# Optimization experiments

Measured on AMD Instinct MI355X. Metric: run time of the kernel, lower is better.

Reference implementation:

```python
import jax, jax.numpy as jnp
import numpy as np

N_NODES = 19
N_T = 4096
LATENT = 512
HID = 2048
N_EDGES = 342


def setup_inputs() -> dict:
    key = jax.random.key(0)
    ks = jax.random.split(key, 16)
    s = lambda fan_in: 1.0 / np.sqrt(fan_in)
    d = {}
    d["latent_z"] = jax.random.normal(ks[0], (N_NODES, LATENT), dtype=jnp.float32)
    d["edge_idx"] = jax.random.randint(ks[1], (2, N_EDGES), 0, N_NODES, dtype=jnp.int64)
    # GIN layer 1 MLP: [LATENT -> HID -> HID]
    d["W1a"] = jax.random.uniform(ks[2], (LATENT, HID), jnp.float32, -s(LATENT), s(LATENT))
    d["b1a"] = jnp.zeros((HID,), jnp.float32)
    d["W1b"] = jax.random.uniform(ks[3], (HID, HID), jnp.float32, -s(HID), s(HID))
    d["b1b"] = jnp.zeros((HID,), jnp.float32)
    # GIN layer 2 MLP: [HID -> N_T -> N_T]
    d["W2a"] = jax.random.uniform(ks[4], (HID, N_T), jnp.float32, -s(HID), s(HID))
    d["b2a"] = jnp.zeros((N_T,), jnp.float32)
    d["W2b"] = jax.random.uniform(ks[5], (N_T, N_T), jnp.float32, -s(N_T), s(N_T))
    d["b2b"] = jnp.zeros((N_T,), jnp.float32)
    # Classifier: Linear(19*4096 -> LATENT), Linear(LATENT -> 1)
    fc_in = N_NODES * N_T
    d["Wc1"] = jax.random.uniform(ks[6], (fc_in, LATENT), jnp.float32, -s(fc_in), s(fc_in))
    d["bc1"] = jnp.zeros((LATENT,), jnp.float32)
    d["Wc2"] = jax.random.uniform(ks[7], (LATENT, 1), jnp.float32, -s(LATENT), s(LATENT))
    d["bc2"] = jnp.zeros((1,), jnp.float32)
    return d


def _gin_agg(h, edge_idx):
    # sum aggregation: message from src (row 0) to dst (row 1); eps = 0
    src, dst = edge_idx[0], edge_idx[1]
    agg = jax.ops.segment_sum(h[src], dst, num_segments=N_NODES)
    return h + agg


def reference(latent_z, edge_idx, W1a, b1a, W1b, b1b, W2a, b2a, W2b, b2b, Wc1, bc1, Wc2, bc2):
    # GINConv 1: nn((1+eps)*x + sum_j x_j), MLP = Lin->ReLU->Lin
    h = _gin_agg(latent_z, edge_idx)
    h = jax.nn.relu(h @ W1a + b1a) @ W1b + b1b
    h = jax.nn.relu(h)  # inter-layer activation (BasicGNN)
    # GINConv 2 (last layer: no trailing activation)
    h = _gin_agg(h, edge_idx)
    gin_recon_signal = jax.nn.relu(h @ W2a + b2a) @ W2b + b2b  # [19, 4096]
    flat = gin_recon_signal.reshape(N_NODES * N_T)
    dem_pred = jax.nn.sigmoid((flat @ Wc1 + bc1) @ Wc2 + bc2)  # [1]
    return (dem_pred, gin_recon_signal)
```

## Files before the change

kernel.cpp:

```cpp
#include <hip/hip_runtime.h>

#define NN 19
#define NT 4096
#define LAT 512
#define HID 2048
#define NE 342

__device__ __forceinline__ void build_M(const int* __restrict__ ei, float* sM,
                                        int* scratch, int t) {
    int* cnt = scratch;
    int* flag = scratch + NN * NN;
    if (t == 0) *flag = 0;
    for (int i = t; i < NN * NN; i += 256) cnt[i] = 0;
    __syncthreads();
    int f = 0;
    for (int i = t; i < NE; i += 256) f |= ei[2 * i + 1];
    if (f) atomicOr(flag, 1);
    __syncthreads();
    const bool i64 = (*flag == 0);
    for (int i = t; i < NE; i += 256) {
        const int s = i64 ? ei[2 * i] : ei[i];
        const int d = i64 ? ei[2 * NE + 2 * i] : ei[NE + i];
        atomicAdd(&cnt[d * NN + s], 1);
    }
    __syncthreads();
    for (int i = t; i < NN * NN; i += 256)
        sM[i] = (float)cnt[i] + ((i / NN) == (i % NN) ? 1.f : 0.f);
    __syncthreads();
}

template <int BK, int N>
__device__ __forceinline__ void gemm_inner(int t, int kc, int cb,
                                           const float* __restrict__ W,
                                           float* __restrict__ part,
                                           const float* __restrict__ sA) {
    const int k0 = kc * BK;
    const int col = cb * 1024 + 4 * t;
    const float4* __restrict__ w = (const float4*)(W + (size_t)k0 * N + col);
    float4 acc[NN];
#pragma unroll
    for (int i = 0; i < NN; ++i) acc[i] = make_float4(0.f, 0.f, 0.f, 0.f);
#pragma unroll 1
    for (int kk = 0; kk < BK; kk += 8) {
        float4 wb[8];
#pragma unroll
        for (int u = 0; u < 8; ++u) wb[u] = w[(size_t)(kk + u) * (N / 4)];
#pragma unroll
        for (int u = 0; u < 8; ++u) {
#pragma unroll
            for (int i = 0; i < NN; ++i) {
                const float av = sA[(kk + u) * 21 + i];
                acc[i].x = fmaf(av, wb[u].x, acc[i].x);
                acc[i].y = fmaf(av, wb[u].y, acc[i].y);
                acc[i].z = fmaf(av, wb[u].z, acc[i].z);
                acc[i].w = fmaf(av, wb[u].w, acc[i].w);
            }
        }
    }
    float* __restrict__ p = part + (size_t)kc * NN * N + col;
#pragma unroll
    for (int i = 0; i < NN; ++i) *(float4*)(p + (size_t)i * N) = acc[i];
}

__global__ __launch_bounds__(256) void gemm_l1a(const float* __restrict__ z,
                                                const int* __restrict__ ei,
                                                const float* __restrict__ W1a,
                                                float* __restrict__ part1) {
    __shared__ __align__(16) float sA[32 * 21];
    __shared__ __align__(16) float sZ[32 * 21];
    __shared__ float sM[NN * NN];
    __shared__ int scratch[NN * NN + 1];
    const int t = threadIdx.x, cb = blockIdx.x, kc = blockIdx.y;
    const int k0 = kc * 32;
    build_M(ei, sM, scratch, t);
    for (int idx = t; idx < NN * 32; idx += 256) {
        const int s = idx / 32, c = idx % 32;
        sZ[c * 21 + s] = z[(size_t)s * LAT + k0 + c];
    }
    __syncthreads();
    for (int idx = t; idx < NN * 32; idx += 256) {
        const int i = idx / 32, c = idx % 32;
        float acc = 0.f;
#pragma unroll
        for (int s = 0; s < NN; ++s) acc = fmaf(sM[i * NN + s], sZ[c * 21 + s], acc);
        sA[c * 21 + i] = acc;
    }
    __syncthreads();
    gemm_inner<32, HID>(t, kc, cb, W1a, part1, sA);
}

__global__ __launch_bounds__(256) void gemm_l1b(const float* __restrict__ part1,
                                                const float* __restrict__ b1a,
                                                const float* __restrict__ W1b,
                                                float* __restrict__ part2) {
    __shared__ __align__(16) float sA[64 * 21];
    const int t = threadIdx.x, cb = blockIdx.x, kc = blockIdx.y;
    const int k0 = kc * 64;
    for (int idx = t; idx < NN * 64; idx += 256) {
        const int i = idx / 64, c = idx % 64;
        const int k = k0 + c;
        float s = b1a[k];
#pragma unroll
        for (int cc = 0; cc < 16; ++cc) s += part1[((size_t)cc * NN + i) * HID + k];
        sA[c * 21 + i] = s > 0.f ? s : 0.f;
    }
    __syncthreads();
    gemm_inner<64, HID>(t, kc, cb, W1b, part2, sA);
}

__global__ __launch_bounds__(256) void gemm_l2a(const float* __restrict__ part2,
                                                const float* __restrict__ b1b,
                                                const int* __restrict__ ei,
                                                const float* __restrict__ W2a,
                                                float* __restrict__ part3) {
    __shared__ __align__(16) float sA[64 * 21];
    __shared__ __align__(16) float sZ[64 * 21];
    __shared__ float sM[NN * NN];
    __shared__ int scratch[NN * NN + 1];
    const int t = threadIdx.x, cb = blockIdx.x, kc = blockIdx.y;
    const int k0 = kc * 64;
    build_M(ei, sM, scratch, t);
    for (int idx = t; idx < NN * 64; idx += 256) {
        const int i = idx / 64, c = idx % 64;
        const int k = k0 + c;
        float s = b1b[k];
#pragma unroll
        for (int cc = 0; cc < 32; ++cc) s += part2[((size_t)cc * NN + i) * HID + k];
        sZ[c * 21 + i] = s > 0.f ? s : 0.f;
    }
    __syncthreads();
    for (int idx = t; idx < NN * 64; idx += 256) {
        const int i = idx / 64, c = idx % 64;
        float acc = 0.f;
#pragma unroll
        for (int s = 0; s < NN; ++s) acc = fmaf(sM[i * NN + s], sZ[c * 21 + s], acc);
        sA[c * 21 + i] = acc;
    }
    __syncthreads();
    gemm_inner<64, NT>(t, kc, cb, W2a, part3, sA);
}

__global__ __launch_bounds__(256) void gemm_l2b(const float* __restrict__ part3,
                                                const float* __restrict__ b2a,
                                                const float* __restrict__ W2b,
                                                float* __restrict__ part4) {
    __shared__ __align__(16) float sA[64 * 21];
    const int t = threadIdx.x, cb = blockIdx.x, kc = blockIdx.y;
    const int k0 = kc * 64;
    for (int idx = t; idx < NN * 64; idx += 256) {
        const int i = idx / 64, c = idx % 64;
        const int k = k0 + c;
        float s = b2a[k];
#pragma unroll
        for (int cc = 0; cc < 32; ++cc) s += part3[((size_t)cc * NN + i) * NT + k];
        sA[c * 21 + i] = s > 0.f ? s : 0.f;
    }
    __syncthreads();
    gemm_inner<64, NT>(t, kc, cb, W2b, part4, sA);
}

__global__ __launch_bounds__(256) void cls_out(const float* __restrict__ part4,
                                               const float* __restrict__ b2b,
                                               const float* __restrict__ Wc1,
                                               float* __restrict__ out1,
                                               float* __restrict__ partC) {
    __shared__ float sF[304];
    __shared__ __align__(16) float4 comb[128];
    const int t = threadIdx.x;
    const int k0 = blockIdx.x * 304;
    for (int e = t; e < 304; e += 256) {
        const int f = k0 + e;
        const int i = f >> 12, n = f & 4095;
        float s = b2b[n];
#pragma unroll 16
        for (int cc = 0; cc < 64; ++cc) s += part4[((size_t)cc * NN + i) * NT + n];
        sF[e] = s;
        out1[f] = s;
    }
    __syncthreads();
    const int q = t & 127, kp = t >> 7;
    const float4* __restrict__ w = (const float4*)Wc1 + (size_t)k0 * 128 + q;
    float4 acc = make_float4(0.f, 0.f, 0.f, 0.f);
#pragma unroll 1
    for (int k = kp; k < 304; k += 16) {
        float4 wb[8];
        float fv[8];
#pragma unroll
        for (int u = 0; u < 8; ++u) wb[u] = w[(size_t)(k + 2 * u) * 128];
#pragma unroll
        for (int u = 0; u < 8; ++u) fv[u] = sF[k + 2 * u];
#pragma unroll
        for (int u = 0; u < 8; ++u) {
            acc.x = fmaf(fv[u], wb[u].x, acc.x);
            acc.y = fmaf(fv[u], wb[u].y, acc.y);
            acc.z = fmaf(fv[u], wb[u].z, acc.z);
            acc.w = fmaf(fv[u], wb[u].w, acc.w);
        }
    }
    if (kp) comb[q] = acc;
    __syncthreads();
    if (!kp) {
        const float4 o = comb[q];
        acc.x += o.x; acc.y += o.y; acc.z += o.z; acc.w += o.w;
        ((float4*)partC)[(size_t)blockIdx.x * 128 + q] = acc;
    }
}

__global__ __launch_bounds__(256) void cls_reduce(const float* __restrict__ partC,
                                                  float* __restrict__ part2c) {
    const int g = blockIdx.x, t = threadIdx.x;
    float2 s = make_float2(0.f, 0.f);
#pragma unroll
    for (int c = 0; c < 16; ++c) {
        const float2 v = *(const float2*)(partC + (size_t)(g * 16 + c) * LAT + 2 * t);
        s.x += v.x; s.y += v.y;
    }
    *(float2*)(part2c + (size_t)g * LAT + 2 * t) = s;
}

__global__ __launch_bounds__(512) void cls_final(const float* __restrict__ part2c,
                                                 const float* __restrict__ bc1,
                                                 const float* __restrict__ Wc2,
                                                 const float* __restrict__ bc2,
                                                 float* __restrict__ out) {
    __shared__ float red[512];
    const int t = threadIdx.x;
    float s = bc1[t];
#pragma unroll
    for (int g = 0; g < 16; ++g) s += part2c[(size_t)g * LAT + t];
    red[t] = s * Wc2[t];
    __syncthreads();
    for (int off = 256; off > 0; off >>= 1) {
        if (t < off) red[t] += red[t + off];
        __syncthreads();
    }
    if (t == 0) out[0] = 1.f / (1.f + expf(-(red[0] + bc2[0])));
}

extern "C" void kernel_launch(void* const* d_in, const int* in_sizes, int n_in,
                              void* d_out, int out_size, void* d_ws, size_t ws_size,
                              hipStream_t stream) {
    const float* z   = (const float*)d_in[0];
    const int*   ei  = (const int*)d_in[1];
    const float* W1a = (const float*)d_in[2];
    const float* b1a = (const float*)d_in[3];
    const float* W1b = (const float*)d_in[4];
    const float* b1b = (const float*)d_in[5];
    const float* W2a = (const float*)d_in[6];
    const float* b2a = (const float*)d_in[7];
    const float* W2b = (const float*)d_in[8];
    const float* b2b = (const float*)d_in[9];
    const float* Wc1 = (const float*)d_in[10];
    const float* bc1 = (const float*)d_in[11];
    const float* Wc2 = (const float*)d_in[12];
    const float* bc2 = (const float*)d_in[13];
    float* out = (float*)d_out;
    float* ws  = (float*)d_ws;

    float* part1  = ws + 262144;
    float* part2  = ws + 1048576;
    float* part3  = ws + 2359296;
    float* part4  = ws + 4980736;
    float* partC  = ws + 10485760;
    float* part2c = ws + 10616832;

    gemm_l1a<<<dim3(2, 16), 256, 0, stream>>>(z, ei, W1a, part1);
    gemm_l1b<<<dim3(2, 32), 256, 0, stream>>>(part1, b1a, W1b, part2);
    gemm_l2a<<<dim3(4, 32), 256, 0, stream>>>(part2, b1b, ei, W2a, part3);
    gemm_l2b<<<dim3(4, 64), 256, 0, stream>>>(part3, b2a, W2b, part4);
    cls_out<<<256, 256, 0, stream>>>(part4, b2b, Wc1, out + 1, partC);
    cls_reduce<<<16, 256, 0, stream>>>(partC, part2c);
    cls_final<<<1, 512, 0, stream>>>(part2c, bc1, Wc2, bc2, out);
}
```

Measured before the change: 157.8 us.

## Fuse layer-1 GEMMs into one kernel and fold classifier reduction into last block

Layer 1's two GEMMs are merged into one 512-thread kernel. Each block computes the full aggregated input, then its 64-column slice of the first hidden layer with a K-split shuffle reduction, then feeds that slice directly into the W1b partial product. This removes the part1 round trip and one launch. The classifier's cls_reduce and cls_final kernels are folded into cls_out through an atomic counter, so the last finishing block does the final reduction and sigmoid, saving two launches. In exchange, each layer-1 block recomputes the full first-layer aggregation (32x redundant) and reads W1a column-strided. The tail also relies on a counter that is reset inside the first kernel.

```diff
diff --git a/kernel.cpp b/kernel.cpp
--- a/kernel.cpp
+++ b/kernel.cpp
@@ -7,35 +7,34 @@
 #define NE 342
 
 __device__ __forceinline__ void build_M(const int* __restrict__ ei, float* sM,
-                                        int* scratch, int t) {
+                                        int* scratch, int t, int bs) {
     int* cnt = scratch;
     int* flag = scratch + NN * NN;
     if (t == 0) *flag = 0;
-    for (int i = t; i < NN * NN; i += 256) cnt[i] = 0;
+    for (int i = t; i < NN * NN; i += bs) cnt[i] = 0;
     __syncthreads();
     int f = 0;
-    for (int i = t; i < NE; i += 256) f |= ei[2 * i + 1];
+    for (int i = t; i < NE; i += bs) f |= ei[2 * i + 1];
     if (f) atomicOr(flag, 1);
     __syncthreads();
     const bool i64 = (*flag == 0);
-    for (int i = t; i < NE; i += 256) {
+    for (int i = t; i < NE; i += bs) {
         const int s = i64 ? ei[2 * i] : ei[i];
         const int d = i64 ? ei[2 * NE + 2 * i] : ei[NE + i];
         atomicAdd(&cnt[d * NN + s], 1);
     }
     __syncthreads();
-    for (int i = t; i < NN * NN; i += 256)
+    for (int i = t; i < NN * NN; i += bs)
         sM[i] = (float)cnt[i] + ((i / NN) == (i % NN) ? 1.f : 0.f);
     __syncthreads();
 }
 
 template <int BK, int N>
-__device__ __forceinline__ void gemm_inner(int t, int kc, int cb,
+__device__ __forceinline__ void gemm_inner(int col, int kc,
                                            const float* __restrict__ W,
                                            float* __restrict__ part,
                                            const float* __restrict__ sA) {
     const int k0 = kc * BK;
-    const int col = cb * 1024 + 4 * t;
     const float4* __restrict__ w = (const float4*)(W + (size_t)k0 * N + col);
     float4 acc[NN];
 #pragma unroll
@@ -62,50 +61,90 @@
     for (int i = 0; i < NN; ++i) *(float4*)(p + (size_t)i * N) = acc[i];
 }
 
-__global__ __launch_bounds__(256) void gemm_l1a(const float* __restrict__ z,
-                                                const int* __restrict__ ei,
-                                                const float* __restrict__ W1a,
-                                                float* __restrict__ part1) {
-    __shared__ __align__(16) float sA[32 * 21];
-    __shared__ __align__(16) float sZ[32 * 21];
+__global__ __launch_bounds__(512) void gemm_l1ab(const float* __restrict__ z,
+                                                 const int* __restrict__ ei,
+                                                 const float* __restrict__ W1a,
+                                                 const float* __restrict__ b1a,
+                                                 const float* __restrict__ W1b,
+                                                 float* __restrict__ part2,
+                                                 unsigned int* __restrict__ counter) {
+    __shared__ __align__(16) float h0T[512 * 20];
+    __shared__ __align__(16) float sA[64 * 21];
     __shared__ float sM[NN * NN];
     __shared__ int scratch[NN * NN + 1];
-    const int t = threadIdx.x, cb = blockIdx.x, kc = blockIdx.y;
-    const int k0 = kc * 32;
-    build_M(ei, sM, scratch, t);
-    for (int idx = t; idx < NN * 32; idx += 256) {
-        const int s = idx / 32, c = idx % 32;
-        sZ[c * 21 + s] = z[(size_t)s * LAT + k0 + c];
-    }
-    __syncthreads();
-    for (int idx = t; idx < NN * 32; idx += 256) {
-        const int i = idx / 32, c = idx % 32;
-        float acc = 0.f;
-#pragma unroll
-        for (int s = 0; s < NN; ++s) acc = fmaf(sM[i * NN + s], sZ[c * 21 + s], acc);
-        sA[c * 21 + i] = acc;
-    }
-    __syncthreads();
-    gemm_inner<32, HID>(t, kc, cb, W1a, part1, sA);
-}
-
-__global__ __launch_bounds__(256) void gemm_l1b(const float* __restrict__ part1,
-                                                const float* __restrict__ b1a,
-                                                const float* __restrict__ W1b,
-                                                float* __restrict__ part2) {
-    __shared__ __align__(16) float sA[64 * 21];
-    const int t = threadIdx.x, cb = blockIdx.x, kc = blockIdx.y;
-    const int k0 = kc * 64;
-    for (int idx = t; idx < NN * 64; idx += 256) {
-        const int i = idx / 64, c = idx % 64;
-        const int k = k0 + c;
-        float s = b1a[k];
-#pragma unroll
-        for (int cc = 0; cc < 16; ++cc) s += part1[((size_t)cc * NN + i) * HID + k];
-        sA[c * 21 + i] = s > 0.f ? s : 0.f;
-    }
-    __syncthreads();
-    gemm_inner<64, HID>(t, kc, cb, W1b, part2, sA);
+    const int t = threadIdx.x;
+    const int kc = blockIdx.x;
+    if (kc == 0 && t == 0) *counter = 0u;
+    build_M(ei, sM, scratch, t, 512);
+    {
+        float zv[NN];
+#pragma unroll
+        for (int s = 0; s < NN; ++s) zv[s] = z[(size_t)s * LAT + t];
+#pragma unroll
+        for (int i = 0; i < NN; ++i) {
+            float a = 0.f;
+#pragma unroll
+            for (int s = 0; s < NN; ++s) a = fmaf(sM[i * NN + s], zv[s], a);
+            h0T[t * 20 + i] = a;
+        }
+    }
+    __syncthreads();
+    {
+        const int c = t >> 3, jp = t & 7;
+        const int k = kc * 64 + c;
+        float acc[NN];
+#pragma unroll
+        for (int i = 0; i < NN; ++i) acc[i] = 0.f;
+#pragma unroll 1
+        for (int jj = 0; jj < 64; jj += 8) {
+            float wv[8];
+#pragma unroll
+            for (int u = 0; u < 8; ++u)
+                wv[u] = W1a[(size_t)(8 * (jj + u) + jp) * HID + k];
+#pragma unroll
+            for (int u = 0; u < 8; ++u) {
+                const float* hr = h0T + (8 * (jj + u) + jp) * 20;
+                const float4 a0 = *(const float4*)(hr);
+                const float4 a1 = *(const float4*)(hr + 4);
+                const float4 a2 = *(const float4*)(hr + 8);
+                const float4 a3 = *(const float4*)(hr + 12);
+                const float4 a4 = *(const float4*)(hr + 16);
+                const float wu = wv[u];
+                acc[0]  = fmaf(a0.x, wu, acc[0]);
+                acc[1]  = fmaf(a0.y, wu, acc[1]);
+                acc[2]  = fmaf(a0.z, wu, acc[2]);
+                acc[3]  = fmaf(a0.w, wu, acc[3]);
+                acc[4]  = fmaf(a1.x, wu, acc[4]);
+                acc[5]  = fmaf(a1.y, wu, acc[5]);
+                acc[6]  = fmaf(a1.z, wu, acc[6]);
+                acc[7]  = fmaf(a1.w, wu, acc[7]);
+                acc[8]  = fmaf(a2.x, wu, acc[8]);
+                acc[9]  = fmaf(a2.y, wu, acc[9]);
+                acc[10] = fmaf(a2.z, wu, acc[10]);
+                acc[11] = fmaf(a2.w, wu, acc[11]);
+                acc[12] = fmaf(a3.x, wu, acc[12]);
+                acc[13] = fmaf(a3.y, wu, acc[13]);
+                acc[14] = fmaf(a3.z, wu, acc[14]);
+                acc[15] = fmaf(a3.w, wu, acc[15]);
+                acc[16] = fmaf(a4.x, wu, acc[16]);
+                acc[17] = fmaf(a4.y, wu, acc[17]);
+                acc[18] = fmaf(a4.z, wu, acc[18]);
+            }
+        }
+#pragma unroll
+        for (int i = 0; i < NN; ++i) {
+            float v = acc[i];
+            v += __shfl_down(v, 1);
+            v += __shfl_down(v, 2);
+            v += __shfl_down(v, 4);
+            if (jp == 0) {
+                const float r = v + b1a[k];
+                sA[c * 21 + i] = r > 0.f ? r : 0.f;
+            }
+        }
+    }
+    __syncthreads();
+    gemm_inner<64, HID>(4 * t, kc, W1b, part2, sA);
 }
 
 __global__ __launch_bounds__(256) void gemm_l2a(const float* __restrict__ part2,
@@ -119,7 +158,7 @@
     __shared__ int scratch[NN * NN + 1];
     const int t = threadIdx.x, cb = blockIdx.x, kc = blockIdx.y;
     const int k0 = kc * 64;
-    build_M(ei, sM, scratch, t);
+    build_M(ei, sM, scratch, t, 256);
     for (int idx = t; idx < NN * 64; idx += 256) {
         const int i = idx / 64, c = idx % 64;
         const int k = k0 + c;
@@ -137,7 +176,7 @@
         sA[c * 21 + i] = acc;
     }
     __syncthreads();
-    gemm_inner<64, NT>(t, kc, cb, W2a, part3, sA);
+    gemm_inner<64, NT>(cb * 1024 + 4 * t, kc, W2a, part3, sA);
 }
 
 __global__ __launch_bounds__(256) void gemm_l2b(const float* __restrict__ part3,
@@ -156,26 +195,33 @@
         sA[c * 21 + i] = s > 0.f ? s : 0.f;
     }
     __syncthreads();
-    gemm_inner<64, NT>(t, kc, cb, W2b, part4, sA);
-}
-
-__global__ __launch_bounds__(256) void cls_out(const float* __restrict__ part4,
-                                               const float* __restrict__ b2b,
-                                               const float* __restrict__ Wc1,
-                                               float* __restrict__ out1,
-                                               float* __restrict__ partC) {
+    gemm_inner<64, NT>(cb * 1024 + 4 * t, kc, W2b, part4, sA);
+}
+
+__global__ __launch_bounds__(256) void cls_out_tail(const float* __restrict__ part4,
+                                                    const float* __restrict__ b2b,
+                                                    const float* __restrict__ Wc1,
+                                                    const float* __restrict__ bc1,
+                                                    const float* __restrict__ Wc2,
+                                                    const float* __restrict__ bc2,
+                                                    float* __restrict__ out,
+                                                    float* __restrict__ partC,
+                                                    unsigned int* __restrict__ counter) {
     __shared__ float sF[304];
     __shared__ __align__(16) float4 comb[128];
+    __shared__ float red[128];
+    __shared__ int lastFlag;
     const int t = threadIdx.x;
     const int k0 = blockIdx.x * 304;
+    float* __restrict__ out1 = out + 1;
     for (int e = t; e < 304; e += 256) {
-        const int f = k0 + e;
-        const int i = f >> 12, n = f & 4095;
+        const int fidx = k0 + e;
+        const int i = fidx >> 12, n = fidx & 4095;
         float s = b2b[n];
 #pragma unroll 16
         for (int cc = 0; cc < 64; ++cc) s += part4[((size_t)cc * NN + i) * NT + n];
         sF[e] = s;
-        out1[f] = s;
+        out1[fidx] = s;
     }
     __syncthreads();
     const int q = t & 127, kp = t >> 7;
@@ -204,33 +250,32 @@
         acc.x += o.x; acc.y += o.y; acc.z += o.z; acc.w += o.w;
         ((float4*)partC)[(size_t)blockIdx.x * 128 + q] = acc;
     }
-}
-
-__global__ __launch_bounds__(256) void cls_reduce(const float* __restrict__ partC,
-                                                  float* __restrict__ part2c) {
-    const int g = blockIdx.x, t = threadIdx.x;
-    float2 s = make_float2(0.f, 0.f);
-#pragma unroll
-    for (int c = 0; c < 16; ++c) {
-        const float2 v = *(const float2*)(partC + (size_t)(g * 16 + c) * LAT + 2 * t);
-        s.x += v.x; s.y += v.y;
-    }
-    *(float2*)(part2c + (size_t)g * LAT + 2 * t) = s;
-}
-
-__global__ __launch_bounds__(512) void cls_final(const float* __restrict__ part2c,
-                                                 const float* __restrict__ bc1,
-                                                 const float* __restrict__ Wc2,
-                                                 const float* __restrict__ bc2,
-                                                 float* __restrict__ out) {
-    __shared__ float red[512];
-    const int t = threadIdx.x;
-    float s = bc1[t];
-#pragma unroll
-    for (int g = 0; g < 16; ++g) s += part2c[(size_t)g * LAT + t];
-    red[t] = s * Wc2[t];
-    __syncthreads();
-    for (int off = 256; off > 0; off >>= 1) {
+    __threadfence();
+    __syncthreads();
+    if (t == 0) lastFlag = (atomicAdd(counter, 1u) == 255u) ? 1 : 0;
+    __syncthreads();
+    if (!lastFlag) return;
+    __threadfence();
+    const int half = kp;
+    float4 s = make_float4(0.f, 0.f, 0.f, 0.f);
+    const float4* __restrict__ pc = (const float4*)partC;
+#pragma unroll 8
+    for (int c = half * 128; c < half * 128 + 128; ++c) {
+        const float4 v = pc[(size_t)c * 128 + q];
+        s.x += v.x; s.y += v.y; s.z += v.z; s.w += v.w;
+    }
+    __syncthreads();
+    if (half) comb[q] = s;
+    __syncthreads();
+    if (!half) {
+        const float4 o = comb[q];
+        const float4 b = ((const float4*)bc1)[q];
+        const float4 w2 = ((const float4*)Wc2)[q];
+        red[t] = (s.x + o.x + b.x) * w2.x + (s.y + o.y + b.y) * w2.y +
+                 (s.z + o.z + b.z) * w2.z + (s.w + o.w + b.w) * w2.w;
+    }
+    __syncthreads();
+    for (int off = 64; off > 0; off >>= 1) {
         if (t < off) red[t] += red[t + off];
         __syncthreads();
     }
@@ -257,18 +302,15 @@
     float* out = (float*)d_out;
     float* ws  = (float*)d_ws;
 
-    float* part1  = ws + 262144;
-    float* part2  = ws + 1048576;
-    float* part3  = ws + 2359296;
-    float* part4  = ws + 4980736;
-    float* partC  = ws + 10485760;
-    float* part2c = ws + 10616832;
-
-    gemm_l1a<<<dim3(2, 16), 256, 0, stream>>>(z, ei, W1a, part1);
-    gemm_l1b<<<dim3(2, 32), 256, 0, stream>>>(part1, b1a, W1b, part2);
+    unsigned int* counter = (unsigned int*)ws;
+    float* part2 = ws + 1048576;
+    float* part3 = ws + 2359296;
+    float* part4 = ws + 4980736;
+    float* partC = ws + 10485760;
+
+    gemm_l1ab<<<32, 512, 0, stream>>>(z, ei, W1a, b1a, W1b, part2, counter);
     gemm_l2a<<<dim3(4, 32), 256, 0, stream>>>(part2, b1b, ei, W2a, part3);
     gemm_l2b<<<dim3(4, 64), 256, 0, stream>>>(part3, b2a, W2b, part4);
-    cls_out<<<256, 256, 0, stream>>>(part4, b2b, Wc1, out + 1, partC);
-    cls_reduce<<<16, 256, 0, stream>>>(partC, part2c);
-    cls_final<<<1, 512, 0, stream>>>(part2c, bc1, Wc2, bc2, out);
-}
+    cls_out_tail<<<256, 256, 0, stream>>>(part4, b2b, Wc1, bc1, Wc2, bc2,
+                                          out, partC, counter);
+}
```

Result: slower. 192.7 us (+22.1%).

## Fuse classifier stages into one kernel with last-block reduction and Wc2 folding

Applied to the files above, without the earlier changes.

Replaces the three classifier kernels with a single kernel over 1024 blocks. Each block sums the part4 partials for 76 features using two thread halves, writes the recon output, and multiplies by Wc1. It then folds the Wc2 dot product in right away, so each block emits one scalar instead of a 512-wide partial. A global atomic counter, reset inside the first GEMM kernel, picks the last block to do the final reduction with bias and sigmoid. This removes two launches and the partial-buffer round trips, and spreads Wc1 streaming over more blocks. The cost is a threadfence/atomic pattern, and launch_bounds minimum-occupancy hints are added to the GEMMs.

```diff
diff --git a/kernel.cpp b/kernel.cpp
--- a/kernel.cpp
+++ b/kernel.cpp
@@ -7,35 +7,34 @@
 #define NE 342
 
 __device__ __forceinline__ void build_M(const int* __restrict__ ei, float* sM,
-                                        int* scratch, int t) {
+                                        int* scratch, int t, int bs) {
     int* cnt = scratch;
     int* flag = scratch + NN * NN;
     if (t == 0) *flag = 0;
-    for (int i = t; i < NN * NN; i += 256) cnt[i] = 0;
+    for (int i = t; i < NN * NN; i += bs) cnt[i] = 0;
     __syncthreads();
     int f = 0;
-    for (int i = t; i < NE; i += 256) f |= ei[2 * i + 1];
+    for (int i = t; i < NE; i += bs) f |= ei[2 * i + 1];
     if (f) atomicOr(flag, 1);
     __syncthreads();
     const bool i64 = (*flag == 0);
-    for (int i = t; i < NE; i += 256) {
+    for (int i = t; i < NE; i += bs) {
         const int s = i64 ? ei[2 * i] : ei[i];
         const int d = i64 ? ei[2 * NE + 2 * i] : ei[NE + i];
         atomicAdd(&cnt[d * NN + s], 1);
     }
     __syncthreads();
-    for (int i = t; i < NN * NN; i += 256)
+    for (int i = t; i < NN * NN; i += bs)
         sM[i] = (float)cnt[i] + ((i / NN) == (i % NN) ? 1.f : 0.f);
     __syncthreads();
 }
 
 template <int BK, int N>
-__device__ __forceinline__ void gemm_inner(int t, int kc, int cb,
+__device__ __forceinline__ void gemm_inner(int col, int kc,
                                            const float* __restrict__ W,
                                            float* __restrict__ part,
                                            const float* __restrict__ sA) {
     const int k0 = kc * BK;
-    const int col = cb * 1024 + 4 * t;
     const float4* __restrict__ w = (const float4*)(W + (size_t)k0 * N + col);
     float4 acc[NN];
 #pragma unroll
@@ -62,17 +61,19 @@
     for (int i = 0; i < NN; ++i) *(float4*)(p + (size_t)i * N) = acc[i];
 }
 
-__global__ __launch_bounds__(256) void gemm_l1a(const float* __restrict__ z,
-                                                const int* __restrict__ ei,
-                                                const float* __restrict__ W1a,
-                                                float* __restrict__ part1) {
+__global__ __launch_bounds__(256, 2) void gemm_l1a(const float* __restrict__ z,
+                                                   const int* __restrict__ ei,
+                                                   const float* __restrict__ W1a,
+                                                   float* __restrict__ part1,
+                                                   unsigned int* __restrict__ counter) {
     __shared__ __align__(16) float sA[32 * 21];
     __shared__ __align__(16) float sZ[32 * 21];
     __shared__ float sM[NN * NN];
     __shared__ int scratch[NN * NN + 1];
     const int t = threadIdx.x, cb = blockIdx.x, kc = blockIdx.y;
     const int k0 = kc * 32;
-    build_M(ei, sM, scratch, t);
+    if (cb == 0 && kc == 0 && t == 0) *counter = 0u;
+    build_M(ei, sM, scratch, t, 256);
     for (int idx = t; idx < NN * 32; idx += 256) {
         const int s = idx / 32, c = idx % 32;
         sZ[c * 21 + s] = z[(size_t)s * LAT + k0 + c];
@@ -86,13 +87,13 @@
         sA[c * 21 + i] = acc;
     }
     __syncthreads();
-    gemm_inner<32, HID>(t, kc, cb, W1a, part1, sA);
-}
-
-__global__ __launch_bounds__(256) void gemm_l1b(const float* __restrict__ part1,
-                                                const float* __restrict__ b1a,
-                                                const float* __restrict__ W1b,
-                                                float* __restrict__ part2) {
+    gemm_inner<32, HID>(cb * 1024 + 4 * t, kc, W1a, part1, sA);
+}
+
+__global__ __launch_bounds__(256, 2) void gemm_l1b(const float* __restrict__ part1,
+                                                   const float* __restrict__ b1a,
+                                                   const float* __restrict__ W1b,
+                                                   float* __restrict__ part2) {
     __shared__ __align__(16) float sA[64 * 21];
     const int t = threadIdx.x, cb = blockIdx.x, kc = blockIdx.y;
     const int k0 = kc * 64;
@@ -105,21 +106,21 @@
         sA[c * 21 + i] = s > 0.f ? s : 0.f;
     }
     __syncthreads();
-    gemm_inner<64, HID>(t, kc, cb, W1b, part2, sA);
-}
-
-__global__ __launch_bounds__(256) void gemm_l2a(const float* __restrict__ part2,
-                                                const float* __restrict__ b1b,
-                                                const int* __restrict__ ei,
-                                                const float* __restrict__ W2a,
-                                                float* __restrict__ part3) {
+    gemm_inner<64, HID>(cb * 1024 + 4 * t, kc, W1b, part2, sA);
+}
+
+__global__ __launch_bounds__(256, 2) void gemm_l2a(const float* __restrict__ part2,
+                                                   const float* __restrict__ b1b,
+                                                   const int* __restrict__ ei,
+                                                   const float* __restrict__ W2a,
+                                                   float* __restrict__ part3) {
     __shared__ __align__(16) float sA[64 * 21];
     __shared__ __align__(16) float sZ[64 * 21];
     __shared__ float sM[NN * NN];
     __shared__ int scratch[NN * NN + 1];
     const int t = threadIdx.x, cb = blockIdx.x, kc = blockIdx.y;
     const int k0 = kc * 64;
-    build_M(ei, sM, scratch, t);
+    build_M(ei, sM, scratch, t, 256);
     for (int idx = t; idx < NN * 64; idx += 256) {
         const int i = idx / 64, c = idx % 64;
         const int k = k0 + c;
@@ -137,13 +138,13 @@
         sA[c * 21 + i] = acc;
     }
     __syncthreads();
-    gemm_inner<64, NT>(t, kc, cb, W2a, part3, sA);
-}
-
-__global__ __launch_bounds__(256) void gemm_l2b(const float* __restrict__ part3,
-                                                const float* __restrict__ b2a,
-                                                const float* __restrict__ W2b,
-                                                float* __restrict__ part4) {
+    gemm_inner<64, NT>(cb * 1024 + 4 * t, kc, W2a, part3, sA);
+}
+
+__global__ __launch_bounds__(256, 2) void gemm_l2b(const float* __restrict__ part3,
+                                                   const float* __restrict__ b2a,
+                                                   const float* __restrict__ W2b,
+                                                   float* __restrict__ part4) {
     __shared__ __align__(16) float sA[64 * 21];
     const int t = threadIdx.x, cb = blockIdx.x, kc = blockIdx.y;
     const int k0 = kc * 64;
@@ -156,81 +157,84 @@
         sA[c * 21 + i] = s > 0.f ? s : 0.f;
     }
     __syncthreads();
-    gemm_inner<64, NT>(t, kc, cb, W2b, part4, sA);
-}
-
-__global__ __launch_bounds__(256) void cls_out(const float* __restrict__ part4,
-                                               const float* __restrict__ b2b,
-                                               const float* __restrict__ Wc1,
-                                               float* __restrict__ out1,
-                                               float* __restrict__ partC) {
-    __shared__ float sF[304];
-    __shared__ __align__(16) float4 comb[128];
+    gemm_inner<64, NT>(cb * 1024 + 4 * t, kc, W2b, part4, sA);
+}
+
+__global__ __launch_bounds__(256, 4) void cls_fused(const float* __restrict__ part4,
+                                                    const float* __restrict__ b2b,
+                                                    const float* __restrict__ Wc1,
+                                                    const float* __restrict__ bc1,
+                                                    const float* __restrict__ Wc2,
+                                                    const float* __restrict__ bc2,
+                                                    float* __restrict__ out,
+                                                    float* __restrict__ scal,
+                                                    unsigned int* __restrict__ counter) {
+    __shared__ float sF[76];
+    __shared__ float red[256];
+    __shared__ int lastFlag;
     const int t = threadIdx.x;
-    const int k0 = blockIdx.x * 304;
-    for (int e = t; e < 304; e += 256) {
-        const int f = k0 + e;
-        const int i = f >> 12, n = f & 4095;
-        float s = b2b[n];
+    const int bid = blockIdx.x;
+    const int k0 = bid * 76;
+
+    const int e = t & 127, h = t >> 7;
+    float partial = 0.f;
+    if (e < 76) {
+        const int fidx = k0 + e;
+        const int i = fidx >> 12, n = fidx & 4095;
+        const float* __restrict__ p = part4 + ((size_t)(h * 32 * NN + i)) * NT + n;
 #pragma unroll 16
-        for (int cc = 0; cc < 64; ++cc) s += part4[((size_t)cc * NN + i) * NT + n];
+        for (int cc = 0; cc < 32; ++cc) partial += p[(size_t)cc * NN * NT];
+    }
+    if (e < 76 && h) red[e] = partial;
+    __syncthreads();
+    if (e < 76 && !h) {
+        const int fidx = k0 + e;
+        const float s = partial + red[e] + b2b[fidx & 4095];
         sF[e] = s;
-        out1[f] = s;
-    }
-    __syncthreads();
-    const int q = t & 127, kp = t >> 7;
-    const float4* __restrict__ w = (const float4*)Wc1 + (size_t)k0 * 128 + q;
-    float4 acc = make_float4(0.f, 0.f, 0.f, 0.f);
+        out[1 + fidx] = s;
+    }
+    __syncthreads();
+
+    const float2* __restrict__ w2 = (const float2*)Wc1 + (size_t)k0 * 256 + t;
+    float accx = 0.f, accy = 0.f;
 #pragma unroll 1
-    for (int k = kp; k < 304; k += 16) {
-        float4 wb[8];
-        float fv[8];
-#pragma unroll
-        for (int u = 0; u < 8; ++u) wb[u] = w[(size_t)(k + 2 * u) * 128];
-#pragma unroll
-        for (int u = 0; u < 8; ++u) fv[u] = sF[k + 2 * u];
-#pragma unroll
-        for (int u = 0; u < 8; ++u) {
-            acc.x = fmaf(fv[u], wb[u].x, acc.x);
-            acc.y = fmaf(fv[u], wb[u].y, acc.y);
-            acc.z = fmaf(fv[u], wb[u].z, acc.z);
-            acc.w = fmaf(fv[u], wb[u].w, acc.w);
+    for (int g = 0; g < 4; ++g) {
+        float2 wb[19];
+        float fv[19];
+#pragma unroll
+        for (int u = 0; u < 19; ++u) wb[u] = w2[(size_t)(g * 19 + u) * 256];
+#pragma unroll
+        for (int u = 0; u < 19; ++u) fv[u] = sF[g * 19 + u];
+#pragma unroll
+        for (int u = 0; u < 19; ++u) {
+            accx = fmaf(fv[u], wb[u].x, accx);
+            accy = fmaf(fv[u], wb[u].y, accy);
         }
     }
-    if (kp) comb[q] = acc;
-    __syncthreads();
-    if (!kp) {
-        const float4 o = comb[q];
-        acc.x += o.x; acc.y += o.y; acc.z += o.z; acc.w += o.w;
-        ((float4*)partC)[(size_t)blockIdx.x * 128 + q] = acc;
-    }
-}
-
-__global__ __launch_bounds__(256) void cls_reduce(const float* __restrict__ partC,
-                                                  float* __restrict__ part2c) {
-    const int g = blockIdx.x, t = threadIdx.x;
-    float2 s = make_float2(0.f, 0.f);
-#pragma unroll
-    for (int c = 0; c < 16; ++c) {
-        const float2 v = *(const float2*)(partC + (size_t)(g * 16 + c) * LAT + 2 * t);
-        s.x += v.x; s.y += v.y;
-    }
-    *(float2*)(part2c + (size_t)g * LAT + 2 * t) = s;
-}
-
-__global__ __launch_bounds__(512) void cls_final(const float* __restrict__ part2c,
-                                                 const float* __restrict__ bc1,
-                                                 const float* __restrict__ Wc2,
-                                                 const float* __restrict__ bc2,
-                                                 float* __restrict__ out) {
-    __shared__ float red[512];
-    const int t = threadIdx.x;
-    float s = bc1[t];
-#pragma unroll
-    for (int g = 0; g < 16; ++g) s += part2c[(size_t)g * LAT + t];
-    red[t] = s * Wc2[t];
-    __syncthreads();
-    for (int off = 256; off > 0; off >>= 1) {
+
+    const float2 wv = ((const float2*)Wc2)[t];
+    red[t] = accx * wv.x + accy * wv.y;
+    __syncthreads();
+    for (int off = 128; off > 0; off >>= 1) {
+        if (t < off) red[t] += red[t + off];
+        __syncthreads();
+    }
+    if (t == 0) scal[bid] = red[0];
+    __threadfence();
+    __syncthreads();
+    if (t == 0) lastFlag = (atomicAdd(counter, 1u) == 1023u) ? 1 : 0;
+    __syncthreads();
+    if (!lastFlag) return;
+    __threadfence();
+
+    float s = 0.f;
+#pragma unroll
+    for (int c = 0; c < 4; ++c) s += scal[t + 256 * c];
+    const float2 b1 = ((const float2*)bc1)[t];
+    s += b1.x * wv.x + b1.y * wv.y;
+    red[t] = s;
+    __syncthreads();
+    for (int off = 128; off > 0; off >>= 1) {
         if (t < off) red[t] += red[t + off];
         __syncthreads();
     }
@@ -257,18 +261,17 @@
     float* out = (float*)d_out;
     float* ws  = (float*)d_ws;
 
-    float* part1  = ws + 262144;
-    float* part2  = ws + 1048576;
-    float* part3  = ws + 2359296;
-    float* part4  = ws + 4980736;
-    float* partC  = ws + 10485760;
-    float* part2c = ws + 10616832;
-
-    gemm_l1a<<<dim3(2, 16), 256, 0, stream>>>(z, ei, W1a, part1);
+    unsigned int* counter = (unsigned int*)ws;
+    float* part1 = ws + 262144;
+    float* part2 = ws + 1048576;
+    float* part3 = ws + 2359296;
+    float* part4 = ws + 4980736;
+    float* scal  = ws + 10485760;
+
+    gemm_l1a<<<dim3(2, 16), 256, 0, stream>>>(z, ei, W1a, part1, counter);
     gemm_l1b<<<dim3(2, 32), 256, 0, stream>>>(part1, b1a, W1b, part2);
     gemm_l2a<<<dim3(4, 32), 256, 0, stream>>>(part2, b1b, ei, W2a, part3);
     gemm_l2b<<<dim3(4, 64), 256, 0, stream>>>(part3, b2a, W2b, part4);
-    cls_out<<<256, 256, 0, stream>>>(part4, b2b, Wc1, out + 1, partC);
-    cls_reduce<<<16, 256, 0, stream>>>(partC, part2c);
-    cls_final<<<1, 512, 0, stream>>>(part2c, bc1, Wc2, bc2, out);
-}
+    cls_fused<<<1024, 256, 0, stream>>>(part4, b2b, Wc1, bc1, Wc2, bc2,
+                                        out, scal, counter);
+}
```

Measured after the change: 298.3 us. 89.0% more time.
